# Optimization experiments

Hardware: AMD Instinct MI355X
Metric: run time of the kernel (lower is better)

The kernel has to match this reference:

```python
import jax, jax.numpy as jnp
import numpy as np

NCE_T = 0.07   # opt.nce_T
EPS = 1e-8     # torch CosineSimilarity eps
DIAG_FILL = -10.0

N, D = 8192, 256

def setup_inputs() -> dict:
    key = jax.random.key(0)
    kq, kk = jax.random.split(key)
    feat_q = jax.random.normal(kq, (N, D), dtype=jnp.float32)
    feat_k = jax.random.normal(kk, (N, D), dtype=jnp.float32)
    return {"feat_q": feat_q, "feat_k": feat_k}

def reference(feat_q, feat_k):
    # feat_k is detached in the original
    feat_k = jax.lax.stop_gradient(feat_k)
    nq = jnp.linalg.norm(feat_q, axis=-1)            # [N]
    nk = jnp.linalg.norm(feat_k, axis=-1)            # [N]
    # positive cosine similarity (paired rows)
    l_pos = jnp.sum(feat_q * feat_k, axis=-1) / jnp.maximum(nq * nk, EPS)  # [N]
    # full N x N cosine similarity via GEMM (torch does a broadcasted version)
    sim = (feat_q @ feat_k.T) / jnp.maximum(nq[:, None] * nk[None, :], EPS)  # [N,N]
    # mask self-similarities with -10.0 BEFORE dividing by temperature
    diag = jnp.eye(sim.shape[0], dtype=bool)
    l_neg = jnp.where(diag, DIAG_FILL, sim)
    out = jnp.concatenate([l_pos[:, None], l_neg], axis=1) / NCE_T  # [N, N+1]
    # cross-entropy vs target class 0, reduction='none'
    loss = jax.scipy.special.logsumexp(out, axis=1) - out[:, 0]     # [N]
    return loss
```

## Files before the change

### kernel.cpp

```cpp
#include <hip/hip_runtime.h>
#include <stdint.h>
#include <math.h>

#define NROWS 8192
#define DDIM  256
#define BM    128
#define BN    128
#define GJ    8
#define COLS_PER_GROUP (NROWS / GJ)

constexpr float INV_T  = 1.0f / 0.07f;
constexpr float LOG2E  = 1.44269504f;
constexpr float K1     = INV_T * LOG2E;

typedef __bf16 bf16x8 __attribute__((ext_vector_type(8)));
typedef float  f32x4  __attribute__((ext_vector_type(4)));

__device__ __forceinline__ void async_copy16(const uint16_t* g, uint16_t* l) {
    __builtin_amdgcn_global_load_lds(
        (const __attribute__((address_space(1))) uint32_t*)g,
        (__attribute__((address_space(3))) uint32_t*)l, 16, 0, 0);
}

__device__ inline uint16_t f2bf(float f) {
    uint32_t u = __float_as_uint(f);
    u += 0x7fffu + ((u >> 16) & 1u);
    return (uint16_t)(u >> 16);
}

__global__ __launch_bounds__(256) void norm_convert_kernel(
    const float* __restrict__ fq, const float* __restrict__ fk,
    uint16_t* __restrict__ qb, uint16_t* __restrict__ kb)
{
    const int wave = threadIdx.x >> 6;
    const int lane = threadIdx.x & 63;
    const int row  = blockIdx.x * 4 + wave;

    const float* src; uint16_t* dstb;
    if (row < NROWS) {
        src = fq + (size_t)row * DDIM; dstb = qb + (size_t)row * DDIM;
    } else {
        int r = row - NROWS;
        src = fk + (size_t)r * DDIM; dstb = kb + (size_t)r * DDIM;
    }

    float4 v = ((const float4*)src)[lane];
    float ss = v.x*v.x + v.y*v.y + v.z*v.z + v.w*v.w;
    #pragma unroll
    for (int m = 1; m < 64; m <<= 1) ss += __shfl_xor(ss, m, 64);
    float r = rsqrtf(ss);

    ushort4 o;
    o.x = f2bf(v.x * r); o.y = f2bf(v.y * r); o.z = f2bf(v.z * r); o.w = f2bf(v.w * r);
    ((ushort4*)dstb)[lane] = o;
}

__global__ __launch_bounds__(256, 2) void nce_main_kernel(
    const uint16_t* __restrict__ qb, const uint16_t* __restrict__ kb,
    float* __restrict__ lpT, float* __restrict__ gpl)
{
    __shared__ __align__(16) uint16_t lds_q[BM * DDIM];
    __shared__ __align__(16) uint16_t lds_k[2 * BN * 32];

    const int tid    = threadIdx.x;
    const int wave   = tid >> 6;
    const int lane   = tid & 63;
    const int quad   = lane >> 4;
    const int lanelo = lane & 15;
    const int wr     = wave >> 1;
    const int wc     = wave & 1;
    const int rowBase      = blockIdx.x * BM;
    const int colGroupBase = blockIdx.y * COLS_PER_GROUP;

    #pragma unroll
    for (int i = 0; i < 16; ++i) {
        int S   = (wave * 16 + i) * 64 + lane;
        int row = S >> 5;
        int ch  = (S & 31) ^ (row & 31);
        async_copy16(qb + (size_t)(rowBase + row) * DDIM + ch * 8,
                     lds_q + (size_t)(wave * 16 + i) * 512);
    }

    int kS0   = wave * 128 + lane;
    int krow0 = kS0 >> 2;
    int kch0  = (lane & 3) ^ ((krow0 >> 1) & 3);
    int krow1 = (kS0 + 64) >> 2;
    int kch1  = (lane & 3) ^ ((krow1 >> 1) & 3);
    const uint16_t* kbase0 = kb + (size_t)(colGroupBase + krow0) * DDIM + kch0 * 8;
    const uint16_t* kbase1 = kb + (size_t)(colGroupBase + krow1) * DDIM + kch1 * 8;
    uint16_t* kl0 = lds_k + wave * 1024;

    async_copy16(kbase0, kl0);
    async_copy16(kbase1, kl0 + 512);
    __syncthreads();

    int rq[4], rq31[4];
    #pragma unroll
    for (int mt = 0; mt < 4; ++mt) {
        rq[mt]   = wr * 64 + mt * 16 + lanelo;
        rq31[mt] = rq[mt] & 31;
    }
    int bvoff[4];
    #pragma unroll
    for (int nt = 0; nt < 4; ++nt) {
        int rk = wc * 64 + nt * 16 + lanelo;
        bvoff[nt] = rk * 32 + (quad ^ ((lanelo >> 1) & 3)) * 8;
    }

    float l_run[16];
    #pragma unroll
    for (int i = 0; i < 16; ++i) l_run[i] = 0.f;

    for (int jt = 0; jt < 8; ++jt) {
        const int colT = colGroupBase + jt * BN;

        f32x4 acc[4][4];
        #pragma unroll
        for (int mt = 0; mt < 4; ++mt)
            #pragma unroll
            for (int nt = 0; nt < 4; ++nt)
                acc[mt][nt] = (f32x4){0.f, 0.f, 0.f, 0.f};

        #pragma unroll
        for (int kk = 0; kk < 8; ++kk) {
            const int p    = (jt << 3) + kk;
            const int buf  = p & 1;
            const int nbuf = buf ^ 1;

            if (p < 63) {
                int np  = p + 1;
                int off = ((np >> 3) << 15) + ((np & 7) << 5);
                uint16_t* ld = lds_k + nbuf * 4096 + wave * 1024;
                async_copy16(kbase0 + off, ld);
                async_copy16(kbase1 + off, ld + 512);
            }

            bf16x8 av[4], bv[4];
            #pragma unroll
            for (int mt = 0; mt < 4; ++mt) {
                int chp = ((kk << 2) + quad) ^ rq31[mt];
                av[mt] = *(const bf16x8*)&lds_q[rq[mt] * 256 + chp * 8];
            }
            #pragma unroll
            for (int nt = 0; nt < 4; ++nt)
                bv[nt] = *(const bf16x8*)&lds_k[buf * 4096 + bvoff[nt]];
            #pragma unroll
            for (int mt = 0; mt < 4; ++mt)
                #pragma unroll
                for (int nt = 0; nt < 4; ++nt)
                    acc[mt][nt] = __builtin_amdgcn_mfma_f32_16x16x32_bf16(av[mt], bv[nt], acc[mt][nt], 0, 0, 0);

            __syncthreads();
        }

        int gcol[4];
        #pragma unroll
        for (int nt = 0; nt < 4; ++nt) gcol[nt] = colT + wc * 64 + nt * 16 + lanelo;
        #pragma unroll
        for (int mt = 0; mt < 4; ++mt) {
            #pragma unroll
            for (int rg = 0; rg < 4; ++rg) {
                int grow = rowBase + wr * 64 + mt * 16 + quad * 4 + rg;
                float s = 0.f;
                #pragma unroll
                for (int nt = 0; nt < 4; ++nt) {
                    float a = acc[mt][nt][rg];
                    float e = exp2f(fmaf(a, K1, -K1));
                    if (grow == gcol[nt]) { lpT[grow] = a * INV_T; e = 0.f; }
                    s += e;
                }
                l_run[mt * 4 + rg] += s;
            }
        }
    }

    #pragma unroll
    for (int i = 0; i < 16; ++i) {
        float v = l_run[i];
        v += __shfl_xor(v, 1, 64);
        v += __shfl_xor(v, 2, 64);
        v += __shfl_xor(v, 4, 64);
        v += __shfl_xor(v, 8, 64);
        l_run[i] = v;
    }
    float* pl = (float*)lds_k;
    if (lanelo == 0) {
        #pragma unroll
        for (int mt = 0; mt < 4; ++mt)
            #pragma unroll
            for (int rg = 0; rg < 4; ++rg) {
                int lr = wr * 64 + mt * 16 + quad * 4 + rg;
                pl[wc * 128 + lr] = l_run[mt * 4 + rg];
            }
    }
    __syncthreads();
    if (tid < 128) {
        float L = pl[tid] + pl[128 + tid];
        gpl[(size_t)blockIdx.y * NROWS + rowBase + tid] = L;
    }
}

__global__ __launch_bounds__(256) void finalize_kernel(
    const float* __restrict__ gpl, const float* __restrict__ lpT,
    float* __restrict__ out)
{
    int t = blockIdx.x * 256 + threadIdx.x;
    if (t >= NROWS) return;
    float L = 0.f;
    #pragma unroll
    for (int g = 0; g < GJ; ++g) L += gpl[g * NROWS + t];
    float lp = lpT[t];
    L += __expf(lp - INV_T);
    out[t] = INV_T + __logf(L) - lp;
}

extern "C" void kernel_launch(void* const* d_in, const int* in_sizes, int n_in,
                              void* d_out, int out_size, void* d_ws, size_t ws_size,
                              hipStream_t stream) {
    const float* fq = (const float*)d_in[0];
    const float* fk = (const float*)d_in[1];
    char* ws = (char*)d_ws;
    uint16_t* qb  = (uint16_t*)(ws);
    uint16_t* kb  = (uint16_t*)(ws + 4194304);
    float*    lpT = (float*)(ws + 8388608);
    float*    gpl = (float*)(ws + 8421376);

    norm_convert_kernel<<<(2 * NROWS) / 4, 256, 0, stream>>>(fq, fk, qb, kb);
    dim3 grid(NROWS / BM, GJ);
    nce_main_kernel<<<grid, 256, 0, stream>>>(qb, kb, lpT, gpl);
    finalize_kernel<<<NROWS / 256, 256, 0, stream>>>(gpl, lpT, (float*)d_out);
}
```

Baseline: 111.5 us.

## Fold positive logit into diagonal, shrink row tile, raise occupancy

The main kernel no longer checks every element for the diagonal. It sums exp over all columns, so the diagonal entry (which equals the positive pair's cosine) stands in for the positive-logit term that finalize used to add. The exact positive logit is now computed in fp32 inside the normalization kernel from q, k norms and their dot product. The row tile drops from 128 to 64 and the launch-bounds occupancy hint rises to 3 blocks. This cuts registers and LDS per block but halves reuse of each loaded K tile and doubles K global traffic.

```diff
diff --git a/kernel.cpp b/kernel.cpp
--- a/kernel.cpp
+++ b/kernel.cpp
@@ -4,7 +4,7 @@
 
 #define NROWS 8192
 #define DDIM  256
-#define BM    128
+#define BM    64
 #define BN    128
 #define GJ    8
 #define COLS_PER_GROUP (NROWS / GJ)
@@ -30,34 +30,52 @@
 
 __global__ __launch_bounds__(256) void norm_convert_kernel(
     const float* __restrict__ fq, const float* __restrict__ fk,
-    uint16_t* __restrict__ qb, uint16_t* __restrict__ kb)
+    uint16_t* __restrict__ qb, uint16_t* __restrict__ kb,
+    float* __restrict__ lpT)
 {
     const int wave = threadIdx.x >> 6;
     const int lane = threadIdx.x & 63;
     const int row  = blockIdx.x * 4 + wave;
 
-    const float* src; uint16_t* dstb;
     if (row < NROWS) {
-        src = fq + (size_t)row * DDIM; dstb = qb + (size_t)row * DDIM;
+        const float* qsrc = fq + (size_t)row * DDIM;
+        const float* ksrc = fk + (size_t)row * DDIM;
+        float4 vq = ((const float4*)qsrc)[lane];
+        float4 vk = ((const float4*)ksrc)[lane];
+        float ssq = vq.x*vq.x + vq.y*vq.y + vq.z*vq.z + vq.w*vq.w;
+        float ssk = vk.x*vk.x + vk.y*vk.y + vk.z*vk.z + vk.w*vk.w;
+        float dqk = vq.x*vk.x + vq.y*vk.y + vq.z*vk.z + vq.w*vk.w;
+        #pragma unroll
+        for (int m = 1; m < 64; m <<= 1) {
+            ssq += __shfl_xor(ssq, m, 64);
+            ssk += __shfl_xor(ssk, m, 64);
+            dqk += __shfl_xor(dqk, m, 64);
+        }
+        float r = rsqrtf(ssq);
+        ushort4 o;
+        o.x = f2bf(vq.x * r); o.y = f2bf(vq.y * r); o.z = f2bf(vq.z * r); o.w = f2bf(vq.w * r);
+        ((ushort4*)(qb + (size_t)row * DDIM))[lane] = o;
+        if (lane == 0) {
+            float denom = fmaxf(sqrtf(ssq) * sqrtf(ssk), 1e-8f);
+            lpT[row] = (dqk / denom) * INV_T;
+        }
     } else {
-        int r = row - NROWS;
-        src = fk + (size_t)r * DDIM; dstb = kb + (size_t)r * DDIM;
-    }
-
-    float4 v = ((const float4*)src)[lane];
-    float ss = v.x*v.x + v.y*v.y + v.z*v.z + v.w*v.w;
-    #pragma unroll
-    for (int m = 1; m < 64; m <<= 1) ss += __shfl_xor(ss, m, 64);
-    float r = rsqrtf(ss);
-
-    ushort4 o;
-    o.x = f2bf(v.x * r); o.y = f2bf(v.y * r); o.z = f2bf(v.z * r); o.w = f2bf(v.w * r);
-    ((ushort4*)dstb)[lane] = o;
-}
-
-__global__ __launch_bounds__(256, 2) void nce_main_kernel(
+        const int r_ = row - NROWS;
+        const float* src = fk + (size_t)r_ * DDIM;
+        float4 v = ((const float4*)src)[lane];
+        float ss = v.x*v.x + v.y*v.y + v.z*v.z + v.w*v.w;
+        #pragma unroll
+        for (int m = 1; m < 64; m <<= 1) ss += __shfl_xor(ss, m, 64);
+        float r = rsqrtf(ss);
+        ushort4 o;
+        o.x = f2bf(v.x * r); o.y = f2bf(v.y * r); o.z = f2bf(v.z * r); o.w = f2bf(v.w * r);
+        ((ushort4*)(kb + (size_t)r_ * DDIM))[lane] = o;
+    }
+}
+
+__global__ __launch_bounds__(256, 3) void nce_main_kernel(
     const uint16_t* __restrict__ qb, const uint16_t* __restrict__ kb,
-    float* __restrict__ lpT, float* __restrict__ gpl)
+    float* __restrict__ gpl)
 {
     __shared__ __align__(16) uint16_t lds_q[BM * DDIM];
     __shared__ __align__(16) uint16_t lds_k[2 * BN * 32];
@@ -73,12 +91,12 @@
     const int colGroupBase = blockIdx.y * COLS_PER_GROUP;
 
     #pragma unroll
-    for (int i = 0; i < 16; ++i) {
-        int S   = (wave * 16 + i) * 64 + lane;
+    for (int i = 0; i < 8; ++i) {
+        int S   = (wave * 8 + i) * 64 + lane;
         int row = S >> 5;
         int ch  = (S & 31) ^ (row & 31);
         async_copy16(qb + (size_t)(rowBase + row) * DDIM + ch * 8,
-                     lds_q + (size_t)(wave * 16 + i) * 512);
+                     lds_q + (size_t)(wave * 8 + i) * 512);
     }
 
     int kS0   = wave * 128 + lane;
@@ -94,10 +112,10 @@
     async_copy16(kbase1, kl0 + 512);
     __syncthreads();
 
-    int rq[4], rq31[4];
-    #pragma unroll
-    for (int mt = 0; mt < 4; ++mt) {
-        rq[mt]   = wr * 64 + mt * 16 + lanelo;
+    int rq[2], rq31[2];
+    #pragma unroll
+    for (int mt = 0; mt < 2; ++mt) {
+        rq[mt]   = wr * 32 + mt * 16 + lanelo;
         rq31[mt] = rq[mt] & 31;
     }
     int bvoff[4];
@@ -107,16 +125,14 @@
         bvoff[nt] = rk * 32 + (quad ^ ((lanelo >> 1) & 3)) * 8;
     }
 
-    float l_run[16];
-    #pragma unroll
-    for (int i = 0; i < 16; ++i) l_run[i] = 0.f;
+    float l_run[8];
+    #pragma unroll
+    for (int i = 0; i < 8; ++i) l_run[i] = 0.f;
 
     for (int jt = 0; jt < 8; ++jt) {
-        const int colT = colGroupBase + jt * BN;
-
-        f32x4 acc[4][4];
-        #pragma unroll
-        for (int mt = 0; mt < 4; ++mt)
+        f32x4 acc[2][4];
+        #pragma unroll
+        for (int mt = 0; mt < 2; ++mt)
             #pragma unroll
             for (int nt = 0; nt < 4; ++nt)
                 acc[mt][nt] = (f32x4){0.f, 0.f, 0.f, 0.f};
@@ -135,9 +151,9 @@
                 async_copy16(kbase1 + off, ld + 512);
             }
 
-            bf16x8 av[4], bv[4];
-            #pragma unroll
-            for (int mt = 0; mt < 4; ++mt) {
+            bf16x8 av[2], bv[4];
+            #pragma unroll
+            for (int mt = 0; mt < 2; ++mt) {
                 int chp = ((kk << 2) + quad) ^ rq31[mt];
                 av[mt] = *(const bf16x8*)&lds_q[rq[mt] * 256 + chp * 8];
             }
@@ -145,7 +161,7 @@
             for (int nt = 0; nt < 4; ++nt)
                 bv[nt] = *(const bf16x8*)&lds_k[buf * 4096 + bvoff[nt]];
             #pragma unroll
-            for (int mt = 0; mt < 4; ++mt)
+            for (int mt = 0; mt < 2; ++mt)
                 #pragma unroll
                 for (int nt = 0; nt < 4; ++nt)
                     acc[mt][nt] = __builtin_amdgcn_mfma_f32_16x16x32_bf16(av[mt], bv[nt], acc[mt][nt], 0, 0, 0);
@@ -153,29 +169,21 @@
             __syncthreads();
         }
 
-        int gcol[4];
-        #pragma unroll
-        for (int nt = 0; nt < 4; ++nt) gcol[nt] = colT + wc * 64 + nt * 16 + lanelo;
-        #pragma unroll
-        for (int mt = 0; mt < 4; ++mt) {
+        #pragma unroll
+        for (int mt = 0; mt < 2; ++mt) {
             #pragma unroll
             for (int rg = 0; rg < 4; ++rg) {
-                int grow = rowBase + wr * 64 + mt * 16 + quad * 4 + rg;
                 float s = 0.f;
                 #pragma unroll
-                for (int nt = 0; nt < 4; ++nt) {
-                    float a = acc[mt][nt][rg];
-                    float e = exp2f(fmaf(a, K1, -K1));
-                    if (grow == gcol[nt]) { lpT[grow] = a * INV_T; e = 0.f; }
-                    s += e;
-                }
+                for (int nt = 0; nt < 4; ++nt)
+                    s += exp2f(fmaf(acc[mt][nt][rg], K1, -K1));
                 l_run[mt * 4 + rg] += s;
             }
         }
     }
 
     #pragma unroll
-    for (int i = 0; i < 16; ++i) {
+    for (int i = 0; i < 8; ++i) {
         float v = l_run[i];
         v += __shfl_xor(v, 1, 64);
         v += __shfl_xor(v, 2, 64);
@@ -186,16 +194,16 @@
     float* pl = (float*)lds_k;
     if (lanelo == 0) {
         #pragma unroll
-        for (int mt = 0; mt < 4; ++mt)
+        for (int mt = 0; mt < 2; ++mt)
             #pragma unroll
             for (int rg = 0; rg < 4; ++rg) {
-                int lr = wr * 64 + mt * 16 + quad * 4 + rg;
-                pl[wc * 128 + lr] = l_run[mt * 4 + rg];
+                int lr = wr * 32 + mt * 16 + quad * 4 + rg;
+                pl[wc * 64 + lr] = l_run[mt * 4 + rg];
             }
     }
     __syncthreads();
-    if (tid < 128) {
-        float L = pl[tid] + pl[128 + tid];
+    if (tid < 64) {
+        float L = pl[tid] + pl[64 + tid];
         gpl[(size_t)blockIdx.y * NROWS + rowBase + tid] = L;
     }
 }
@@ -209,9 +217,7 @@
     float L = 0.f;
     #pragma unroll
     for (int g = 0; g < GJ; ++g) L += gpl[g * NROWS + t];
-    float lp = lpT[t];
-    L += __expf(lp - INV_T);
-    out[t] = INV_T + __logf(L) - lp;
+    out[t] = INV_T + __logf(L) - lpT[t];
 }
 
 extern "C" void kernel_launch(void* const* d_in, const int* in_sizes, int n_in,
@@ -225,8 +231,8 @@
     float*    lpT = (float*)(ws + 8388608);
     float*    gpl = (float*)(ws + 8421376);
 
-    norm_convert_kernel<<<(2 * NROWS) / 4, 256, 0, stream>>>(fq, fk, qb, kb);
+    norm_convert_kernel<<<(2 * NROWS) / 4, 256, 0, stream>>>(fq, fk, qb, kb, lpT);
     dim3 grid(NROWS / BM, GJ);
-    nce_main_kernel<<<grid, 256, 0, stream>>>(qb, kb, lpT, gpl);
+    nce_main_kernel<<<grid, 256, 0, stream>>>(qb, kb, gpl);
     finalize_kernel<<<NROWS / 256, 256, 0, stream>>>(gpl, lpT, (float*)d_out);
 }
```

After: 125.8 us. 1.13x slower.
